# Performance work log

Measured on AMD Instinct MI355X. Metric: run time of the kernel, lower is better.

The kernel has to match this reference:

```python
import jax, jax.numpy as jnp
import numpy as np

L, B, S, H, NH, NS = 4, 8, 2048, 1024, 2, 32
DH = H // NH


def _ln(x, g, b, eps):
    m = jnp.mean(x, axis=-1, keepdims=True)
    v = jnp.mean((x - m) ** 2, axis=-1, keepdims=True)
    return (x - m) / jnp.sqrt(v + eps) * g + b


def setup_inputs() -> dict:
    key = jax.random.key(0)
    ks = jax.random.split(key, 8)
    sc = 0.02
    hidden_states = jax.random.normal(ks[0], (L, B, S, H), jnp.float32)
    attention_mask = jnp.ones((B, S), jnp.int32)
    bnd = jnp.sort(jax.random.randint(ks[1], (B, NS + 1), 0, S - 1), axis=1)
    span_head_idxs = bnd[:, :-1]
    span_tail_idxs = jnp.maximum(bnd[:, 1:], span_head_idxs + 1)  # tail > head, <= S-... (S-1+1=S ok since slice end)
    return {
        "hidden_states": hidden_states,
        "attention_mask": attention_mask,
        "span_head_idxs": span_head_idxs,
        "span_tail_idxs": span_tail_idxs,
        "layer_weights": jnp.linspace(-5.0, 5.0, L),
        "ln1_g": jnp.ones((H,)), "ln1_b": jnp.zeros((H,)),
        "Wq": jax.random.normal(ks[2], (H, H)) * sc, "bq": jnp.zeros((H,)),
        "Wk": jax.random.normal(ks[3], (H, H)) * sc, "bk": jnp.zeros((H,)),
        "Wv": jax.random.normal(ks[4], (H, H)) * sc, "bv": jnp.zeros((H,)),
        "Wo": jax.random.normal(ks[5], (H, H)) * sc, "bo": jnp.zeros((H,)),
        "ln2_g": jnp.ones((H,)), "ln2_b": jnp.zeros((H,)),
    }


def reference(hidden_states, attention_mask, span_head_idxs, span_tail_idxs,
              layer_weights, ln1_g, ln1_b, Wq, bq, Wk, bk, Wv, bv, Wo, bo,
              ln2_g, ln2_b):
    l, b, s, h = hidden_states.shape
    # weighted layer average
    w = jax.nn.softmax(layer_weights)                      # [L]
    x = jnp.einsum('l,lbsh->bsh', w, hidden_states)        # [B,S,H]
    # extended mask (additive)
    ext = (1.0 - attention_mask.astype(x.dtype))[:, None, None, :] * -10000.0
    x = _ln(x, ln1_g, ln1_b, 1e-7)
    # BertSelfAttention (dropout = identity in eval)
    q = (x @ Wq.T + bq).reshape(b, s, NH, DH)
    k = (x @ Wk.T + bk).reshape(b, s, NH, DH)
    v = (x @ Wv.T + bv).reshape(b, s, NH, DH)
    scores = jnp.einsum('bqnd,bknd->bnqk', q, k) / jnp.sqrt(jnp.asarray(DH, x.dtype))
    probs = jax.nn.softmax(scores + ext, axis=-1)          # [B,NH,S,S]
    ctx = jnp.einsum('bnqk,bknd->bqnd', probs, v).reshape(b, s, h)
    # BertSelfOutput: dense + residual + LN (eps=1e-12 default)
    y = _ln(ctx @ Wo.T + bo + x, ln2_g, ln2_b, 1e-12)      # [B,S,H]
    # ragged per-span mean via exclusive cumsum
    csum = jnp.concatenate([jnp.zeros((b, 1, h), y.dtype), jnp.cumsum(y, axis=1)], axis=1)  # [B,S+1,H]
    sh = jnp.take_along_axis(csum, span_head_idxs[..., None], axis=1)   # [B,NS,H]
    st = jnp.take_along_axis(csum, span_tail_idxs[..., None], axis=1)
    lengths = (span_tail_idxs - span_head_idxs).astype(y.dtype)[..., None]
    return (st - sh) / lengths
```

## Files before the change

### kernel.cpp

```cpp
#include <hip/hip_runtime.h>
#include <stdint.h>

#define Ln 4
#define Bn 8
#define Sn 2048
#define Hn 1024
#define NHn 2
#define DHn 512
#define NSn 32
#define Mn (Bn*Sn)

typedef __attribute__((ext_vector_type(8))) short bf16x8;
typedef __attribute__((ext_vector_type(4))) float f32x4;
typedef unsigned short u16;

__device__ __forceinline__ float bf2f(u16 u){
  union { unsigned int i; float f; } c; c.i = ((unsigned int)u)<<16; return c.f;
}
__device__ __forceinline__ u16 f2bf(float f){
  union { float f; unsigned int i; } c; c.f = f;
  unsigned int r = c.i + 0x7FFFu + ((c.i>>16)&1u);
  return (u16)(r>>16);
}
__device__ __forceinline__ uint32_t packbf(float a, float b){
  return (uint32_t)f2bf(a) | ((uint32_t)f2bf(b)<<16);
}
__device__ __forceinline__ void gl2lds16(const void* g, void* l){
  __builtin_amdgcn_global_load_lds((const __attribute__((address_space(1))) void*)g,
                                   (__attribute__((address_space(3))) void*)l, 16, 0, 0);
}

__device__ __forceinline__ float block_sum256(float v, float* red){
#pragma unroll
  for (int m=32;m>=1;m>>=1) v += __shfl_xor(v, m, 64);
  int tid = threadIdx.x;
  if ((tid&63)==0) red[tid>>6] = v;
  __syncthreads();
  v = red[0]+red[1]+red[2]+red[3];
  __syncthreads();
  return v;
}

__global__ __launch_bounds__(256) void convw_kernel(const float* __restrict__ Wq, const float* __restrict__ Wk,
    const float* __restrict__ Wv, const float* __restrict__ Wo, u16* __restrict__ wb){
  int m = blockIdx.y;
  const float* src = (m==0)?Wq:(m==1)?Wk:(m==2)?Wv:Wo;
  size_t i = ((size_t)blockIdx.x*256 + threadIdx.x)*4;
  const float4 v = *(const float4*)&src[i];
  ushort4 o;
  o.x=f2bf(v.x); o.y=f2bf(v.y); o.z=f2bf(v.z); o.w=f2bf(v.w);
  *(ushort4*)&wb[(size_t)m*Hn*Hn + i] = o;
}

__global__ __launch_bounds__(256) void mixln_kernel(const float* __restrict__ hs, const float* __restrict__ lw,
    const float* __restrict__ g, const float* __restrict__ be, u16* __restrict__ xb){
  __shared__ float red[4];
  int row = blockIdx.x;
  int tid = threadIdx.x;
  float l0=lw[0], l1=lw[1], l2=lw[2], l3=lw[3];
  float mx = fmaxf(fmaxf(l0,l1),fmaxf(l2,l3));
  float e0=__expf(l0-mx), e1=__expf(l1-mx), e2=__expf(l2-mx), e3=__expf(l3-mx);
  float inv = 1.0f/(e0+e1+e2+e3);
  e0*=inv; e1*=inv; e2*=inv; e3*=inv;
  size_t base = (size_t)row*Hn + tid*4;
  const float4 h0 = *(const float4*)&hs[base];
  const float4 h1 = *(const float4*)&hs[base + (size_t)Mn*Hn];
  const float4 h2 = *(const float4*)&hs[base + (size_t)2*Mn*Hn];
  const float4 h3 = *(const float4*)&hs[base + (size_t)3*Mn*Hn];
  float x0 = e0*h0.x + e1*h1.x + e2*h2.x + e3*h3.x;
  float x1 = e0*h0.y + e1*h1.y + e2*h2.y + e3*h3.y;
  float x2 = e0*h0.z + e1*h1.z + e2*h2.z + e3*h3.z;
  float x3 = e0*h0.w + e1*h1.w + e2*h2.w + e3*h3.w;
  float s = block_sum256(x0+x1+x2+x3, red);
  float mean = s * (1.0f/Hn);
  float d0=x0-mean, d1=x1-mean, d2=x2-mean, d3=x3-mean;
  float sq = block_sum256(d0*d0+d1*d1+d2*d2+d3*d3, red);
  float rstd = rsqrtf(sq*(1.0f/Hn) + 1e-7f);
  int c = tid*4;
  ushort4 o;
  o.x = f2bf(d0*rstd*g[c+0] + be[c+0]);
  o.y = f2bf(d1*rstd*g[c+1] + be[c+1]);
  o.z = f2bf(d2*rstd*g[c+2] + be[c+2]);
  o.w = f2bf(d3*rstd*g[c+3] + be[c+3]);
  *(ushort4*)&xb[(size_t)row*Hn + c] = o;
}

template<int MODE>
__global__ __launch_bounds__(512,2) void gemm256_kernel(const u16* __restrict__ A, const u16* __restrict__ Bw,
    const float* __restrict__ bias, const u16* __restrict__ resid, void* __restrict__ Cout, float scale){
  __shared__ char ldsb[131072];
  int tid = threadIdx.x, lane = tid&63, wid = tid>>6;
  int ln = lane&15, g4 = lane>>4;
  int wm = wid>>2, wn = wid&3;
  int swz = (blockIdx.x&7)*32 + (blockIdx.x>>3);
  int i0 = (swz>>2)*256;
  int j0 = (swz&3)*256;

  f32x4 acc[8][4];
#pragma unroll
  for (int a=0;a<8;a++)
#pragma unroll
    for (int b=0;b<4;b++) acc[a][b] = (f32x4){0.f,0.f,0.f,0.f};

  const u16* Asrc = A + (size_t)i0*Hn;
  const u16* Bsrc = Bw + (size_t)j0*Hn;
  const int hA = wm, hB = wn>>1, bB = (wn&1)*64;

#define LDSOFF(B,AB,H) ((((B)*2+(AB))*2+(H))*16384)
#define STG(AB,H,B,T) do { \
    const u16* s_ = (AB) ? Bsrc : Asrc; \
    char* d_ = ldsb + LDSOFF(B,AB,H); \
    _Pragma("unroll") \
    for (int l_=0;l_<2;++l_){ \
      int g_ = l_*512 + tid; int r_ = g_>>3; int cs_ = (g_&7) ^ (r_&7); \
      gl2lds16(s_ + (size_t)((H)*128 + r_)*Hn + (T)*64 + cs_*8, d_ + g_*16); \
    } } while(0)
#define RDH(B,AB,H,RR,KG) (*(const bf16x8*)(ldsb + LDSOFF(B,AB,H) + (RR)*128 + ((((KG)) ^ ((RR)&7))<<4)))
#define LOADA(B,I) { _Pragma("unroll") for (int mt=0;mt<4;++mt) \
    _Pragma("unroll") for (int kk=0;kk<2;++kk) af[mt][kk] = RDH(B,0,hA,(I)*64+mt*16+ln, kk*4+g4); }
#define LOADB(B,ARR,J) { _Pragma("unroll") for (int nt=0;nt<2;++nt) \
    _Pragma("unroll") for (int kk=0;kk<2;++kk) ARR[nt][kk] = RDH(B,1,hB, bB+((J)*2+nt)*16+ln, kk*4+g4); }
#define PH_OPEN __builtin_amdgcn_s_barrier(); \
    asm volatile("s_waitcnt lgkmcnt(0)" ::: "memory"); \
    __builtin_amdgcn_sched_barrier(0);
#define MM(I,J,BF) { __builtin_amdgcn_s_setprio(1); \
    _Pragma("unroll") for (int kk=0;kk<2;++kk) \
    _Pragma("unroll") for (int mt=0;mt<4;++mt) \
    _Pragma("unroll") for (int nt=0;nt<2;++nt) \
      acc[(I)*4+mt][(J)*2+nt] = __builtin_amdgcn_mfma_f32_16x16x32_bf16(af[mt][kk], BF[nt][kk], acc[(I)*4+mt][(J)*2+nt], 0,0,0); \
    __builtin_amdgcn_s_setprio(0); }
#define PH_CLOSE __builtin_amdgcn_s_barrier();

  STG(0,0,0,0); STG(0,1,0,0); STG(1,0,0,0); STG(1,1,0,0);
  STG(0,0,1,1);
  asm volatile("s_waitcnt vmcnt(2)" ::: "memory");
  __builtin_amdgcn_s_barrier();

  bf16x8 af[4][2], bf0[2][2], bf1[2][2];
#pragma unroll 1
  for (int it=0; it<8; ++it){
    const int u = 2*it, v = 2*it+1;
    const bool st = (it < 7);
    LOADA(0,0); LOADB(0,bf0,0);
    STG(0,1,1,v);
    PH_OPEN; MM(0,0,bf0); PH_CLOSE;
    LOADB(0,bf1,1);
    STG(1,0,1,v);
    PH_OPEN; MM(0,1,bf1); PH_CLOSE;
    LOADA(0,1);
    STG(1,1,1,v);
    PH_OPEN; MM(1,0,bf0); PH_CLOSE;
    if (st) STG(0,0,0,u+2);
    PH_OPEN; MM(1,1,bf1);
    if (st) { asm volatile("s_waitcnt vmcnt(2)" ::: "memory"); }
    else    { asm volatile("s_waitcnt vmcnt(0)" ::: "memory"); }
    PH_CLOSE;
    LOADA(1,0); LOADB(1,bf0,0);
    if (st) STG(0,1,0,u+2);
    PH_OPEN; MM(0,0,bf0); PH_CLOSE;
    LOADB(1,bf1,1);
    if (st) STG(1,0,0,u+2);
    PH_OPEN; MM(0,1,bf1); PH_CLOSE;
    LOADA(1,1);
    if (st) STG(1,1,0,u+2);
    PH_OPEN; MM(1,0,bf0); PH_CLOSE;
    if (st) STG(0,0,1,v+2);
    PH_OPEN; MM(1,1,bf1);
    if (st) { asm volatile("s_waitcnt vmcnt(2)" ::: "memory"); }
    else    { asm volatile("s_waitcnt vmcnt(0)" ::: "memory"); }
    PH_CLOSE;
  }
#undef LDSOFF
#undef STG
#undef RDH
#undef LOADA
#undef LOADB
#undef PH_OPEN
#undef MM
#undef PH_CLOSE

#pragma unroll
  for (int mt=0; mt<8; ++mt){
#pragma unroll
    for (int nt=0; nt<4; ++nt){
#pragma unroll
      for (int r=0; r<4; ++r){
        int i = i0 + wm*128 + mt*16 + g4*4 + r;
        int j = j0 + wn*64 + nt*16 + ln;
        float v = acc[mt][nt][r] + bias[j];
        if (MODE==0){
          int b = i>>11, s = i&2047, nh = j>>9, dh = j&511;
          ((u16*)Cout)[(((size_t)(b*NHn+nh)*Sn + s)<<9) + dh] = f2bf(v*scale);
        } else if (MODE==1){
          int b = i>>11, s = i&2047, nh = j>>9, dh = j&511;
          ((u16*)Cout)[((size_t)((b*NHn+nh)*(Sn/32) + (s>>5))<<14) + (dh<<5) + (s&31)] = f2bf(v);
        } else {
          float res = bf2f(resid[(size_t)i*Hn + j]);
          ((u16*)Cout)[(size_t)i*Hn + j] = f2bf(v + res);
        }
      }
    }
  }
}

__global__ __launch_bounds__(512,2) void attn_kernel(const u16* __restrict__ qb, const u16* __restrict__ kb,
    const u16* __restrict__ vt, const int* __restrict__ mask, u16* __restrict__ ctx){
  __shared__ u16 Ks[2][32*512];
  __shared__ u16 Vs[2][512*32];
  __shared__ u16 Ps[8*16*32];
  __shared__ float Lcorr[128];
  __shared__ float Lflag[8];
  __shared__ float Linv[128];
  int tid = threadIdx.x, lane = tid&63, wid = tid>>6;
  int ln = lane&15, g4 = lane>>4;
  int gid = blockIdx.x;
  int xcd = gid&7, ord = gid>>3;
  int bh = xcd*2 + (ord>>4), qt = ord&15;
  int b = bh >> 1, nh = bh & 1;
  u16* pw = Ps + wid*512;
  uint32_t* pw32 = (uint32_t*)pw;
  const int swz = (ln&7)<<4;
  const int rsw = (ln>>1)&3;

  bf16x8 aq[16];
  size_t qoff = ((size_t)bh*Sn + qt*128 + wid*16 + ln)*DHn + g4*8;
#pragma unroll
  for (int ch=0; ch<16; ++ch) aq[ch] = *(const bf16x8*)&qb[qoff + ch*32];

  f32x4 o2[8][4];
#pragma unroll
  for (int qf=0; qf<8; ++qf)
#pragma unroll
    for (int df=0; df<4; ++df) o2[qf][df] = (f32x4){0.f,0.f,0.f,0.f};
  float mrun = -1e30f, lrun = 0.f;

  const size_t kbase = (size_t)bh*Sn*DHn;
  const u16* vtile = vt + (size_t)bh*Sn*DHn;

#define STAGE_KV(KT,BUF) do { \
  _Pragma("unroll") \
  for (int t_=0; t_<4; ++t_){ \
    int krow_ = t_*8 + wid; \
    int koff_ = (lane*16) ^ ((krow_&7)<<4); \
    gl2lds16(&kb[kbase + ((size_t)((KT)*32 + krow_))*DHn + (koff_>>1)], \
             (char*)Ks[BUF] + krow_*1024 + lane*16); \
  } \
  _Pragma("unroll") \
  for (int t_=0; t_<4; ++t_){ \
    int p_ = t_*512 + tid; \
    int cgd_ = ((p_&3) ^ ((p_>>3)&3)); \
    gl2lds16(&vtile[(size_t)(KT)*16384 + (p_&~3)*8 + cgd_*8], \
             (char*)Vs[BUF] + p_*16); \
  } } while(0)

  STAGE_KV(0,0);
  __syncthreads();
#pragma unroll 1
  for (int kt=0; kt<Sn/32; ++kt){
    int cur = kt&1;
    if (kt < Sn/32 - 1) STAGE_KV(kt+1, cur^1);
    const char* KsB = (const char*)Ks[cur];
    f32x4 s0 = (f32x4){0.f,0.f,0.f,0.f};
    f32x4 s1 = (f32x4){0.f,0.f,0.f,0.f};
#pragma unroll
    for (int ch=0; ch<16; ++ch){
      bf16x8 k0 = *(const bf16x8*)(KsB + ln*1024      + ((ch*64 + g4*16) ^ swz));
      bf16x8 k1 = *(const bf16x8*)(KsB + (16+ln)*1024 + ((ch*64 + g4*16) ^ swz));
      s0 = __builtin_amdgcn_mfma_f32_16x16x32_bf16(k0, aq[ch], s0, 0,0,0);
      s1 = __builtin_amdgcn_mfma_f32_16x16x32_bf16(k1, aq[ch], s1, 0,0,0);
    }
    int4 mk0 = *(const int4*)&mask[b*Sn + kt*32 + g4*4];
    int4 mk1 = *(const int4*)&mask[b*Sn + kt*32 + 16 + g4*4];
    s0[0] += (float)(1-mk0.x)*-10000.0f; s0[1] += (float)(1-mk0.y)*-10000.0f;
    s0[2] += (float)(1-mk0.z)*-10000.0f; s0[3] += (float)(1-mk0.w)*-10000.0f;
    s1[0] += (float)(1-mk1.x)*-10000.0f; s1[1] += (float)(1-mk1.y)*-10000.0f;
    s1[2] += (float)(1-mk1.z)*-10000.0f; s1[3] += (float)(1-mk1.w)*-10000.0f;
    float tmax = fmaxf(fmaxf(fmaxf(s0[0],s0[1]),fmaxf(s0[2],s0[3])),
                       fmaxf(fmaxf(s1[0],s1[1]),fmaxf(s1[2],s1[3])));
    tmax = fmaxf(tmax, __shfl_xor(tmax, 16));
    tmax = fmaxf(tmax, __shfl_xor(tmax, 32));
    float corr = 1.0f, wflag = 0.0f;
    if (__any(tmax > mrun + 8.0f)){
      float nm = fmaxf(mrun, tmax);
      corr = __expf(mrun - nm);
      mrun = nm; lrun *= corr;
      wflag = 1.0f;
    }
    float p0=__expf(s0[0]-mrun), p1=__expf(s0[1]-mrun), p2=__expf(s0[2]-mrun), p3=__expf(s0[3]-mrun);
    float p4=__expf(s1[0]-mrun), p5=__expf(s1[1]-mrun), p6=__expf(s1[2]-mrun), p7=__expf(s1[3]-mrun);
    float sum = ((p0+p1)+(p2+p3)) + ((p4+p5)+(p6+p7));
    sum += __shfl_xor(sum, 16);
    sum += __shfl_xor(sum, 32);
    lrun += sum;
    {
      int base = ln*16 + ((g4&1)<<1);
      pw32[base + (((g4>>1)    ^rsw)<<2)    ] = packbf(p0,p1);
      pw32[base + (((g4>>1)    ^rsw)<<2) + 1] = packbf(p2,p3);
      pw32[base + ((((g4>>1)+2)^rsw)<<2)    ] = packbf(p4,p5);
      pw32[base + ((((g4>>1)+2)^rsw)<<2) + 1] = packbf(p6,p7);
    }
    if (lane < 16) Lcorr[wid*16 + ln] = corr;
    if (lane == 0) Lflag[wid] = wflag;
    __builtin_amdgcn_sched_barrier(0);
    asm volatile("s_waitcnt lgkmcnt(0)" ::: "memory");
    __builtin_amdgcn_s_barrier();
    __builtin_amdgcn_sched_barrier(0);
    {
      f32x4 fl0 = *(const f32x4*)&Lflag[0];
      f32x4 fl1 = *(const f32x4*)&Lflag[4];
      float fs = (fl0[0]+fl0[1]+fl0[2]+fl0[3]) + (fl1[0]+fl1[1]+fl1[2]+fl1[3]);
      if (fs > 0.5f){
#pragma unroll
        for (int qf=0; qf<8; ++qf){
          f32x4 c4 = *(const f32x4*)&Lcorr[qf*16 + g4*4];
#pragma unroll
          for (int df=0; df<4; ++df){
            o2[qf][df][0]*=c4[0]; o2[qf][df][1]*=c4[1];
            o2[qf][df][2]*=c4[2]; o2[qf][df][3]*=c4[3];
          }
        }
      }
    }
    const char* VsB = (const char*)Vs[cur];
    bf16x8 bv[4];
#pragma unroll
    for (int df=0; df<4; ++df)
      bv[df] = *(const bf16x8*)(VsB + ((wid*4+df)*16+ln)*64 + ((g4 ^ rsw)<<4));
#pragma unroll
    for (int qf=0; qf<8; ++qf){
      bf16x8 aP = *(const bf16x8*)&Ps[qf*512 + ln*32 + ((g4 ^ rsw)<<3)];
#pragma unroll
      for (int df=0; df<4; ++df)
        o2[qf][df] = __builtin_amdgcn_mfma_f32_16x16x32_bf16(aP, bv[df], o2[qf][df], 0,0,0);
    }
    __syncthreads();
  }
#undef STAGE_KV
  if (lane < 16) Linv[wid*16 + ln] = 1.0f/lrun;
  __syncthreads();
  int qr0 = qt*128;
#pragma unroll
  for (int qf=0; qf<8; ++qf){
    f32x4 il4 = *(const f32x4*)&Linv[qf*16 + g4*4];
#pragma unroll
    for (int df=0; df<4; ++df){
#pragma unroll
      for (int r=0; r<4; ++r){
        int q = qr0 + qf*16 + g4*4 + r;
        int d = nh*DHn + wid*64 + df*16 + ln;
        ctx[((size_t)(b*Sn + q))*Hn + d] = f2bf(o2[qf][df][r]*il4[r]);
      }
    }
  }
}

__global__ __launch_bounds__(256) void ln2_kernel(u16* __restrict__ t, const float* __restrict__ g,
    const float* __restrict__ be){
  __shared__ float red[4];
  int row = blockIdx.x, tid = threadIdx.x;
  const ushort4 xu = *(const ushort4*)&t[(size_t)row*Hn + tid*4];
  float x0 = bf2f(xu.x), x1 = bf2f(xu.y), x2 = bf2f(xu.z), x3 = bf2f(xu.w);
  float s = block_sum256(x0+x1+x2+x3, red);
  float mean = s*(1.0f/Hn);
  float d0=x0-mean, d1=x1-mean, d2=x2-mean, d3=x3-mean;
  float sq = block_sum256(d0*d0+d1*d1+d2*d2+d3*d3, red);
  float rstd = rsqrtf(sq*(1.0f/Hn) + 1e-12f);
  int c = tid*4;
  ushort4 y;
  y.x = f2bf(d0*rstd*g[c+0] + be[c+0]);
  y.y = f2bf(d1*rstd*g[c+1] + be[c+1]);
  y.z = f2bf(d2*rstd*g[c+2] + be[c+2]);
  y.w = f2bf(d3*rstd*g[c+3] + be[c+3]);
  *(ushort4*)&t[(size_t)row*Hn + c] = y;
}

__global__ __launch_bounds__(256) void span_kernel(const u16* __restrict__ y, const int* __restrict__ head,
    const int* __restrict__ tail, float* __restrict__ out){
  int bs = blockIdx.x;
  int b = bs >> 5;
  int hd = head[bs], tl = tail[bs];
  int c = threadIdx.x*4;
  float a0=0.f,a1=0.f,a2=0.f,a3=0.f;
  for (int s=hd; s<tl; ++s){
    const ushort4 v = *(const ushort4*)&y[((size_t)(b*Sn + s))*Hn + c];
    a0+=bf2f(v.x); a1+=bf2f(v.y); a2+=bf2f(v.z); a3+=bf2f(v.w);
  }
  float inv = 1.0f/(float)(tl-hd);
  float4 o; o.x=a0*inv; o.y=a1*inv; o.z=a2*inv; o.w=a3*inv;
  *(float4*)&out[(size_t)bs*Hn + c] = o;
}

extern "C" void kernel_launch(void* const* d_in, const int* in_sizes, int n_in,
                              void* d_out, int out_size, void* d_ws, size_t ws_size,
                              hipStream_t stream) {
  const float* hs    = (const float*)d_in[0];
  const int*   mask  = (const int*)d_in[1];
  const int*   shead = (const int*)d_in[2];
  const int*   stail = (const int*)d_in[3];
  const float* lw    = (const float*)d_in[4];
  const float* ln1g  = (const float*)d_in[5];
  const float* ln1b  = (const float*)d_in[6];
  const float* Wq    = (const float*)d_in[7];
  const float* bq    = (const float*)d_in[8];
  const float* Wk    = (const float*)d_in[9];
  const float* bk    = (const float*)d_in[10];
  const float* Wv    = (const float*)d_in[11];
  const float* bv    = (const float*)d_in[12];
  const float* Wo    = (const float*)d_in[13];
  const float* bo    = (const float*)d_in[14];
  const float* ln2g  = (const float*)d_in[15];
  const float* ln2b  = (const float*)d_in[16];

  char* ws = (char*)d_ws;
  u16* xb  = (u16*)(ws);
  u16* wb  = (u16*)(ws + 33554432);
  u16* qb  = (u16*)(ws + 41943040);
  u16* kb  = (u16*)(ws + 75497472);
  u16* vt  = (u16*)(ws + 109051904);
  u16* ctx = (u16*)(ws + 142606336);
  u16* t   = (u16*)(ws + 41943040);
  float* out = (float*)d_out;

  convw_kernel<<<dim3(1024,4),256,0,stream>>>(Wq,Wk,Wv,Wo,wb);
  mixln_kernel<<<Mn,256,0,stream>>>(hs,lw,ln1g,ln1b,xb);
  gemm256_kernel<0><<<256,512,0,stream>>>(xb, wb,           bq, nullptr, qb, 0.044194173824159223f);
  gemm256_kernel<0><<<256,512,0,stream>>>(xb, wb+1048576,   bk, nullptr, kb, 1.0f);
  gemm256_kernel<1><<<256,512,0,stream>>>(xb, wb+2097152,   bv, nullptr, vt, 1.0f);
  attn_kernel<<<256,512,0,stream>>>(qb,kb,vt,mask,ctx);
  gemm256_kernel<2><<<256,512,0,stream>>>(ctx, wb+3145728,  bo, xb, t, 1.0f);
  ln2_kernel<<<Mn,256,0,stream>>>(t, ln2g, ln2b);
  span_kernel<<<Bn*NSn,256,0,stream>>>(t, shead, stail, out);
}
```

Measured before the change: 547.4 us.

## Fuse QKV projections into one GEMM launch and widen attention key tiles to 64

The three Q/K/V projection GEMMs become a single 768-block launch. Each block picks its bias, scale and output layout from the column tile it owns, which removes two launches and fills the GPU with more concurrent tiles. The attention kernel now processes 64 keys per iteration instead of 32. K staging is no longer double-buffered: the next K tile is issued after the mid-iteration barrier, and V is staged at the start of the same iteration. This halves the loop trip count and barrier count per key, at the cost of less load/compute overlap and larger P/K LDS buffers.

Result: slower. 654.5 us (+19.6%).

```diff
diff --git a/kernel.cpp b/kernel.cpp
--- a/kernel.cpp
+++ b/kernel.cpp
@@ -87,14 +87,22 @@
 
 template<int MODE>
 __global__ __launch_bounds__(512,2) void gemm256_kernel(const u16* __restrict__ A, const u16* __restrict__ Bw,
-    const float* __restrict__ bias, const u16* __restrict__ resid, void* __restrict__ Cout, float scale){
+    const float* __restrict__ b0, const float* __restrict__ b1, const float* __restrict__ b2,
+    const u16* __restrict__ resid, void* __restrict__ Cout, float scale){
   __shared__ char ldsb[131072];
   int tid = threadIdx.x, lane = tid&63, wid = tid>>6;
   int ln = lane&15, g4 = lane>>4;
   int wm = wid>>2, wn = wid&3;
-  int swz = (blockIdx.x&7)*32 + (blockIdx.x>>3);
-  int i0 = (swz>>2)*256;
-  int j0 = (swz&3)*256;
+  int i0, j0;
+  if (MODE==0){
+    int xcd = blockIdx.x&7, idx = blockIdx.x>>3;
+    i0 = (xcd*8 + idx/12)*256;
+    j0 = (idx%12)*256;
+  } else {
+    int swz = (blockIdx.x&7)*32 + (blockIdx.x>>3);
+    i0 = (swz>>2)*256;
+    j0 = (swz&3)*256;
+  }
 
   f32x4 acc[8][4];
 #pragma unroll
@@ -179,6 +187,10 @@
 #undef MM
 #undef PH_CLOSE
 
+  int mat = (MODE==0) ? (j0>>10) : 0;
+  const float* bias = (MODE==0) ? ((mat==0)?b0:((mat==1)?b1:b2)) : b0;
+  float sc = (MODE==0 && mat==0) ? scale : 1.0f;
+  u16* dst = (u16*)Cout + ((MODE==0) ? (size_t)mat*16777216 : 0);
 #pragma unroll
   for (int mt=0; mt<8; ++mt){
 #pragma unroll
@@ -187,16 +199,18 @@
       for (int r=0; r<4; ++r){
         int i = i0 + wm*128 + mt*16 + g4*4 + r;
         int j = j0 + wn*64 + nt*16 + ln;
-        float v = acc[mt][nt][r] + bias[j];
+        int jj = j & 1023;
+        float v = acc[mt][nt][r] + bias[jj];
         if (MODE==0){
-          int b = i>>11, s = i&2047, nh = j>>9, dh = j&511;
-          ((u16*)Cout)[(((size_t)(b*NHn+nh)*Sn + s)<<9) + dh] = f2bf(v*scale);
-        } else if (MODE==1){
-          int b = i>>11, s = i&2047, nh = j>>9, dh = j&511;
-          ((u16*)Cout)[((size_t)((b*NHn+nh)*(Sn/32) + (s>>5))<<14) + (dh<<5) + (s&31)] = f2bf(v);
+          int b = i>>11, s = i&2047, nh = jj>>9, dh = jj&511;
+          if (mat < 2){
+            dst[(((size_t)(b*NHn+nh)*Sn + s)<<9) + dh] = f2bf(v*sc);
+          } else {
+            dst[((size_t)((b*NHn+nh)*(Sn/32) + (s>>5))<<14) + (dh<<5) + (s&31)] = f2bf(v);
+          }
         } else {
-          float res = bf2f(resid[(size_t)i*Hn + j]);
-          ((u16*)Cout)[(size_t)i*Hn + j] = f2bf(v + res);
+          float res = bf2f(resid[(size_t)i*Hn + jj]);
+          dst[(size_t)i*Hn + jj] = f2bf(v + res);
         }
       }
     }
@@ -205,9 +219,9 @@
 
 __global__ __launch_bounds__(512,2) void attn_kernel(const u16* __restrict__ qb, const u16* __restrict__ kb,
     const u16* __restrict__ vt, const int* __restrict__ mask, u16* __restrict__ ctx){
-  __shared__ u16 Ks[2][32*512];
+  __shared__ u16 Ks[64*512];
   __shared__ u16 Vs[2][512*32];
-  __shared__ u16 Ps[8*16*32];
+  __shared__ u16 Ps[128*64];
   __shared__ float Lcorr[128];
   __shared__ float Lflag[8];
   __shared__ float Linv[128];
@@ -217,10 +231,10 @@
   int xcd = gid&7, ord = gid>>3;
   int bh = xcd*2 + (ord>>4), qt = ord&15;
   int b = bh >> 1, nh = bh & 1;
-  u16* pw = Ps + wid*512;
-  uint32_t* pw32 = (uint32_t*)pw;
-  const int swz = (ln&7)<<4;
-  const int rsw = (ln>>1)&3;
+  uint32_t* ps32 = (uint32_t*)Ps;
+  const int swz  = (ln&7)<<4;
+  const int rsw  = (ln>>1)&3;
+  const int rsw7 = (ln>>1)&7;
 
   bf16x8 aq[16];
   size_t qoff = ((size_t)bh*Sn + qt*128 + wid*16 + ln)*DHn + g4*8;
@@ -237,46 +251,66 @@
   const size_t kbase = (size_t)bh*Sn*DHn;
   const u16* vtile = vt + (size_t)bh*Sn*DHn;
 
-#define STAGE_KV(KT,BUF) do { \
+#define STAGE_K64(KT) do { \
   _Pragma("unroll") \
-  for (int t_=0; t_<4; ++t_){ \
+  for (int t_=0; t_<8; ++t_){ \
     int krow_ = t_*8 + wid; \
     int koff_ = (lane*16) ^ ((krow_&7)<<4); \
-    gl2lds16(&kb[kbase + ((size_t)((KT)*32 + krow_))*DHn + (koff_>>1)], \
-             (char*)Ks[BUF] + krow_*1024 + lane*16); \
-  } \
+    gl2lds16(&kb[kbase + ((size_t)((KT)*64 + krow_))*DHn + (koff_>>1)], \
+             (char*)Ks + krow_*1024 + lane*16); \
+  } } while(0)
+
+#define STAGE_V64(KT) do { \
   _Pragma("unroll") \
-  for (int t_=0; t_<4; ++t_){ \
-    int p_ = t_*512 + tid; \
-    int cgd_ = ((p_&3) ^ ((p_>>3)&3)); \
-    gl2lds16(&vtile[(size_t)(KT)*16384 + (p_&~3)*8 + cgd_*8], \
-             (char*)Vs[BUF] + p_*16); \
-  } } while(0)
-
-  STAGE_KV(0,0);
+  for (int sub_=0; sub_<2; ++sub_){ \
+    _Pragma("unroll") \
+    for (int t_=0; t_<4; ++t_){ \
+      int p_ = t_*512 + tid; \
+      int cgd_ = ((p_&3) ^ ((p_>>3)&3)); \
+      gl2lds16(&vtile[(size_t)((KT)*2+sub_)*16384 + (p_&~3)*8 + cgd_*8], \
+               (char*)Vs[sub_] + p_*16); \
+    } } } while(0)
+
+  STAGE_K64(0);
   __syncthreads();
 #pragma unroll 1
-  for (int kt=0; kt<Sn/32; ++kt){
-    int cur = kt&1;
-    if (kt < Sn/32 - 1) STAGE_KV(kt+1, cur^1);
-    const char* KsB = (const char*)Ks[cur];
+  for (int kt=0; kt<Sn/64; ++kt){
+    STAGE_V64(kt);
     f32x4 s0 = (f32x4){0.f,0.f,0.f,0.f};
     f32x4 s1 = (f32x4){0.f,0.f,0.f,0.f};
+    f32x4 s2 = (f32x4){0.f,0.f,0.f,0.f};
+    f32x4 s3 = (f32x4){0.f,0.f,0.f,0.f};
 #pragma unroll
     for (int ch=0; ch<16; ++ch){
-      bf16x8 k0 = *(const bf16x8*)(KsB + ln*1024      + ((ch*64 + g4*16) ^ swz));
-      bf16x8 k1 = *(const bf16x8*)(KsB + (16+ln)*1024 + ((ch*64 + g4*16) ^ swz));
+      int co = (ch*64 + g4*16) ^ swz;
+      bf16x8 k0 = *(const bf16x8*)((char*)Ks + (ln   )*1024 + co);
+      bf16x8 k1 = *(const bf16x8*)((char*)Ks + (16+ln)*1024 + co);
+      bf16x8 k2 = *(const bf16x8*)((char*)Ks + (32+ln)*1024 + co);
+      bf16x8 k3 = *(const bf16x8*)((char*)Ks + (48+ln)*1024 + co);
       s0 = __builtin_amdgcn_mfma_f32_16x16x32_bf16(k0, aq[ch], s0, 0,0,0);
       s1 = __builtin_amdgcn_mfma_f32_16x16x32_bf16(k1, aq[ch], s1, 0,0,0);
-    }
-    int4 mk0 = *(const int4*)&mask[b*Sn + kt*32 + g4*4];
-    int4 mk1 = *(const int4*)&mask[b*Sn + kt*32 + 16 + g4*4];
-    s0[0] += (float)(1-mk0.x)*-10000.0f; s0[1] += (float)(1-mk0.y)*-10000.0f;
-    s0[2] += (float)(1-mk0.z)*-10000.0f; s0[3] += (float)(1-mk0.w)*-10000.0f;
-    s1[0] += (float)(1-mk1.x)*-10000.0f; s1[1] += (float)(1-mk1.y)*-10000.0f;
-    s1[2] += (float)(1-mk1.z)*-10000.0f; s1[3] += (float)(1-mk1.w)*-10000.0f;
+      s2 = __builtin_amdgcn_mfma_f32_16x16x32_bf16(k2, aq[ch], s2, 0,0,0);
+      s3 = __builtin_amdgcn_mfma_f32_16x16x32_bf16(k3, aq[ch], s3, 0,0,0);
+    }
+    {
+      int mb = b*Sn + kt*64 + g4*4;
+      int4 mk0 = *(const int4*)&mask[mb];
+      int4 mk1 = *(const int4*)&mask[mb+16];
+      int4 mk2 = *(const int4*)&mask[mb+32];
+      int4 mk3 = *(const int4*)&mask[mb+48];
+      s0[0]+=(float)(1-mk0.x)*-10000.0f; s0[1]+=(float)(1-mk0.y)*-10000.0f;
+      s0[2]+=(float)(1-mk0.z)*-10000.0f; s0[3]+=(float)(1-mk0.w)*-10000.0f;
+      s1[0]+=(float)(1-mk1.x)*-10000.0f; s1[1]+=(float)(1-mk1.y)*-10000.0f;
+      s1[2]+=(float)(1-mk1.z)*-10000.0f; s1[3]+=(float)(1-mk1.w)*-10000.0f;
+      s2[0]+=(float)(1-mk2.x)*-10000.0f; s2[1]+=(float)(1-mk2.y)*-10000.0f;
+      s2[2]+=(float)(1-mk2.z)*-10000.0f; s2[3]+=(float)(1-mk2.w)*-10000.0f;
+      s3[0]+=(float)(1-mk3.x)*-10000.0f; s3[1]+=(float)(1-mk3.y)*-10000.0f;
+      s3[2]+=(float)(1-mk3.z)*-10000.0f; s3[3]+=(float)(1-mk3.w)*-10000.0f;
+    }
     float tmax = fmaxf(fmaxf(fmaxf(s0[0],s0[1]),fmaxf(s0[2],s0[3])),
                        fmaxf(fmaxf(s1[0],s1[1]),fmaxf(s1[2],s1[3])));
+    tmax = fmaxf(tmax, fmaxf(fmaxf(fmaxf(s2[0],s2[1]),fmaxf(s2[2],s2[3])),
+                             fmaxf(fmaxf(s3[0],s3[1]),fmaxf(s3[2],s3[3]))));
     tmax = fmaxf(tmax, __shfl_xor(tmax, 16));
     tmax = fmaxf(tmax, __shfl_xor(tmax, 32));
     float corr = 1.0f, wflag = 0.0f;
@@ -286,25 +320,43 @@
       mrun = nm; lrun *= corr;
       wflag = 1.0f;
     }
-    float p0=__expf(s0[0]-mrun), p1=__expf(s0[1]-mrun), p2=__expf(s0[2]-mrun), p3=__expf(s0[3]-mrun);
-    float p4=__expf(s1[0]-mrun), p5=__expf(s1[1]-mrun), p6=__expf(s1[2]-mrun), p7=__expf(s1[3]-mrun);
-    float sum = ((p0+p1)+(p2+p3)) + ((p4+p5)+(p6+p7));
+    float sum = 0.f;
+    int pbase = (wid*16 + ln)*32 + (g4&1)*2;
+    {
+      float a0=__expf(s0[0]-mrun), a1=__expf(s0[1]-mrun), a2=__expf(s0[2]-mrun), a3=__expf(s0[3]-mrun);
+      sum += (a0+a1)+(a2+a3);
+      int gsw = ((0*2 + (g4>>1)) ^ rsw7)<<2;
+      ps32[pbase + gsw    ] = packbf(a0,a1);
+      ps32[pbase + gsw + 1] = packbf(a2,a3);
+    }
+    {
+      float a0=__expf(s1[0]-mrun), a1=__expf(s1[1]-mrun), a2=__expf(s1[2]-mrun), a3=__expf(s1[3]-mrun);
+      sum += (a0+a1)+(a2+a3);
+      int gsw = ((1*2 + (g4>>1)) ^ rsw7)<<2;
+      ps32[pbase + gsw    ] = packbf(a0,a1);
+      ps32[pbase + gsw + 1] = packbf(a2,a3);
+    }
+    {
+      float a0=__expf(s2[0]-mrun), a1=__expf(s2[1]-mrun), a2=__expf(s2[2]-mrun), a3=__expf(s2[3]-mrun);
+      sum += (a0+a1)+(a2+a3);
+      int gsw = ((2*2 + (g4>>1)) ^ rsw7)<<2;
+      ps32[pbase + gsw    ] = packbf(a0,a1);
+      ps32[pbase + gsw + 1] = packbf(a2,a3);
+    }
+    {
+      float a0=__expf(s3[0]-mrun), a1=__expf(s3[1]-mrun), a2=__expf(s3[2]-mrun), a3=__expf(s3[3]-mrun);
+      sum += (a0+a1)+(a2+a3);
+      int gsw = ((3*2 + (g4>>1)) ^ rsw7)<<2;
+      ps32[pbase + gsw    ] = packbf(a0,a1);
+      ps32[pbase + gsw + 1] = packbf(a2,a3);
+    }
     sum += __shfl_xor(sum, 16);
     sum += __shfl_xor(sum, 32);
     lrun += sum;
-    {
-      int base = ln*16 + ((g4&1)<<1);
-      pw32[base + (((g4>>1)    ^rsw)<<2)    ] = packbf(p0,p1);
-      pw32[base + (((g4>>1)    ^rsw)<<2) + 1] = packbf(p2,p3);
-      pw32[base + ((((g4>>1)+2)^rsw)<<2)    ] = packbf(p4,p5);
-      pw32[base + ((((g4>>1)+2)^rsw)<<2) + 1] = packbf(p6,p7);
-    }
     if (lane < 16) Lcorr[wid*16 + ln] = corr;
     if (lane == 0) Lflag[wid] = wflag;
-    __builtin_amdgcn_sched_barrier(0);
-    asm volatile("s_waitcnt lgkmcnt(0)" ::: "memory");
-    __builtin_amdgcn_s_barrier();
-    __builtin_amdgcn_sched_barrier(0);
+    __syncthreads();
+    if (kt < Sn/64 - 1) STAGE_K64(kt+1);
     {
       f32x4 fl0 = *(const f32x4*)&Lflag[0];
       f32x4 fl1 = *(const f32x4*)&Lflag[4];
@@ -321,21 +373,26 @@
         }
       }
     }
-    const char* VsB = (const char*)Vs[cur];
-    bf16x8 bv[4];
+    bf16x8 bv[4][2];
 #pragma unroll
     for (int df=0; df<4; ++df)
-      bv[df] = *(const bf16x8*)(VsB + ((wid*4+df)*16+ln)*64 + ((g4 ^ rsw)<<4));
+#pragma unroll
+      for (int kc=0; kc<2; ++kc)
+        bv[df][kc] = *(const bf16x8*)((char*)Vs[kc] + ((wid*4+df)*16+ln)*64 + ((g4 ^ rsw)<<4));
 #pragma unroll
     for (int qf=0; qf<8; ++qf){
-      bf16x8 aP = *(const bf16x8*)&Ps[qf*512 + ln*32 + ((g4 ^ rsw)<<3)];
-#pragma unroll
-      for (int df=0; df<4; ++df)
-        o2[qf][df] = __builtin_amdgcn_mfma_f32_16x16x32_bf16(aP, bv[df], o2[qf][df], 0,0,0);
+#pragma unroll
+      for (int kc=0; kc<2; ++kc){
+        bf16x8 aP = *(const bf16x8*)((char*)Ps + (qf*16+ln)*128 + (((kc*4+g4) ^ rsw7)<<4));
+#pragma unroll
+        for (int df=0; df<4; ++df)
+          o2[qf][df] = __builtin_amdgcn_mfma_f32_16x16x32_bf16(aP, bv[df][kc], o2[qf][df], 0,0,0);
+      }
     }
     __syncthreads();
   }
-#undef STAGE_KV
+#undef STAGE_K64
+#undef STAGE_V64
   if (lane < 16) Linv[wid*16 + ln] = 1.0f/lrun;
   __syncthreads();
   int qr0 = qt*128;
@@ -423,11 +480,9 @@
 
   convw_kernel<<<dim3(1024,4),256,0,stream>>>(Wq,Wk,Wv,Wo,wb);
   mixln_kernel<<<Mn,256,0,stream>>>(hs,lw,ln1g,ln1b,xb);
-  gemm256_kernel<0><<<256,512,0,stream>>>(xb, wb,           bq, nullptr, qb, 0.044194173824159223f);
-  gemm256_kernel<0><<<256,512,0,stream>>>(xb, wb+1048576,   bk, nullptr, kb, 1.0f);
-  gemm256_kernel<1><<<256,512,0,stream>>>(xb, wb+2097152,   bv, nullptr, vt, 1.0f);
+  gemm256_kernel<0><<<768,512,0,stream>>>(xb, wb, bq, bk, bv, nullptr, qb, 0.044194173824159223f);
   attn_kernel<<<256,512,0,stream>>>(qb,kb,vt,mask,ctx);
-  gemm256_kernel<2><<<256,512,0,stream>>>(ctx, wb+3145728,  bo, xb, t, 1.0f);
+  gemm256_kernel<2><<<256,512,0,stream>>>(ctx, wb+3145728, bo, bo, bo, xb, t, 1.0f);
   ln2_kernel<<<Mn,256,0,stream>>>(t, ln2g, ln2b);
   span_kernel<<<Bn*NSn,256,0,stream>>>(t, shead, stail, out);
 }
```

## Shrink attention tiles to 64 queries and single-buffer K/V with split staging

Applied to the files above, without the earlier changes.

Attention blocks now cover 64 query rows with 4 waves instead of 128 rows with 8 waves, and the grid doubles to 512 blocks. K and V lose their double buffers. V for the current tile is loaded at the start of the iteration, and K for the next tile is loaded after the mid-loop barrier. The smaller LDS footprint should allow more resident blocks per CU and improve occupancy. In exchange, each block now re-reads K/V for only half as many queries, doubling K/V global traffic, and loads now overlap less with compute.

Result: slower. 777.7 us (+42.1%).

```diff
diff --git a/kernel.cpp b/kernel.cpp
--- a/kernel.cpp
+++ b/kernel.cpp
@@ -203,19 +203,19 @@
   }
 }
 
-__global__ __launch_bounds__(512,2) void attn_kernel(const u16* __restrict__ qb, const u16* __restrict__ kb,
+__global__ __launch_bounds__(256,2) void attn_kernel(const u16* __restrict__ qb, const u16* __restrict__ kb,
     const u16* __restrict__ vt, const int* __restrict__ mask, u16* __restrict__ ctx){
-  __shared__ u16 Ks[2][32*512];
-  __shared__ u16 Vs[2][512*32];
-  __shared__ u16 Ps[8*16*32];
-  __shared__ float Lcorr[128];
-  __shared__ float Lflag[8];
-  __shared__ float Linv[128];
+  __shared__ u16 Ks[32*512];
+  __shared__ u16 Vs[512*32];
+  __shared__ u16 Ps[4*16*32];
+  __shared__ float Lcorr[64];
+  __shared__ float Lflag[4];
+  __shared__ float Linv[64];
   int tid = threadIdx.x, lane = tid&63, wid = tid>>6;
   int ln = lane&15, g4 = lane>>4;
   int gid = blockIdx.x;
   int xcd = gid&7, ord = gid>>3;
-  int bh = xcd*2 + (ord>>4), qt = ord&15;
+  int bh = xcd*2 + (ord>>5), qt = ord&31;
   int b = bh >> 1, nh = bh & 1;
   u16* pw = Ps + wid*512;
   uint32_t* pw32 = (uint32_t*)pw;
@@ -223,49 +223,51 @@
   const int rsw = (ln>>1)&3;
 
   bf16x8 aq[16];
-  size_t qoff = ((size_t)bh*Sn + qt*128 + wid*16 + ln)*DHn + g4*8;
+  size_t qoff = ((size_t)bh*Sn + qt*64 + wid*16 + ln)*DHn + g4*8;
 #pragma unroll
   for (int ch=0; ch<16; ++ch) aq[ch] = *(const bf16x8*)&qb[qoff + ch*32];
 
-  f32x4 o2[8][4];
-#pragma unroll
-  for (int qf=0; qf<8; ++qf)
-#pragma unroll
-    for (int df=0; df<4; ++df) o2[qf][df] = (f32x4){0.f,0.f,0.f,0.f};
+  f32x4 o2[4][8];
+#pragma unroll
+  for (int qf=0; qf<4; ++qf)
+#pragma unroll
+    for (int df=0; df<8; ++df) o2[qf][df] = (f32x4){0.f,0.f,0.f,0.f};
   float mrun = -1e30f, lrun = 0.f;
 
   const size_t kbase = (size_t)bh*Sn*DHn;
   const u16* vtile = vt + (size_t)bh*Sn*DHn;
 
-#define STAGE_KV(KT,BUF) do { \
+#define STAGE_K32(KT) do { \
   _Pragma("unroll") \
-  for (int t_=0; t_<4; ++t_){ \
-    int krow_ = t_*8 + wid; \
+  for (int t_=0; t_<8; ++t_){ \
+    int krow_ = t_*4 + wid; \
     int koff_ = (lane*16) ^ ((krow_&7)<<4); \
     gl2lds16(&kb[kbase + ((size_t)((KT)*32 + krow_))*DHn + (koff_>>1)], \
-             (char*)Ks[BUF] + krow_*1024 + lane*16); \
-  } \
+             (char*)Ks + krow_*1024 + lane*16); \
+  } } while(0)
+
+#define STAGE_V32(KT) do { \
   _Pragma("unroll") \
-  for (int t_=0; t_<4; ++t_){ \
-    int p_ = t_*512 + tid; \
+  for (int t_=0; t_<8; ++t_){ \
+    int p_ = t_*256 + tid; \
     int cgd_ = ((p_&3) ^ ((p_>>3)&3)); \
     gl2lds16(&vtile[(size_t)(KT)*16384 + (p_&~3)*8 + cgd_*8], \
-             (char*)Vs[BUF] + p_*16); \
+             (char*)Vs + p_*16); \
   } } while(0)
 
-  STAGE_KV(0,0);
+  STAGE_K32(0);
   __syncthreads();
 #pragma unroll 1
   for (int kt=0; kt<Sn/32; ++kt){
-    int cur = kt&1;
-    if (kt < Sn/32 - 1) STAGE_KV(kt+1, cur^1);
-    const char* KsB = (const char*)Ks[cur];
+    STAGE_V32(kt);
+    const char* KsB = (const char*)Ks;
     f32x4 s0 = (f32x4){0.f,0.f,0.f,0.f};
     f32x4 s1 = (f32x4){0.f,0.f,0.f,0.f};
 #pragma unroll
     for (int ch=0; ch<16; ++ch){
-      bf16x8 k0 = *(const bf16x8*)(KsB + ln*1024      + ((ch*64 + g4*16) ^ swz));
-      bf16x8 k1 = *(const bf16x8*)(KsB + (16+ln)*1024 + ((ch*64 + g4*16) ^ swz));
+      int co = (ch*64 + g4*16) ^ swz;
+      bf16x8 k0 = *(const bf16x8*)(KsB + ln*1024      + co);
+      bf16x8 k1 = *(const bf16x8*)(KsB + (16+ln)*1024 + co);
       s0 = __builtin_amdgcn_mfma_f32_16x16x32_bf16(k0, aq[ch], s0, 0,0,0);
       s1 = __builtin_amdgcn_mfma_f32_16x16x32_bf16(k1, aq[ch], s1, 0,0,0);
     }
@@ -301,53 +303,51 @@
     }
     if (lane < 16) Lcorr[wid*16 + ln] = corr;
     if (lane == 0) Lflag[wid] = wflag;
-    __builtin_amdgcn_sched_barrier(0);
-    asm volatile("s_waitcnt lgkmcnt(0)" ::: "memory");
-    __builtin_amdgcn_s_barrier();
-    __builtin_amdgcn_sched_barrier(0);
+    __syncthreads();
+    if (kt < Sn/32 - 1) STAGE_K32(kt+1);
     {
-      f32x4 fl0 = *(const f32x4*)&Lflag[0];
-      f32x4 fl1 = *(const f32x4*)&Lflag[4];
-      float fs = (fl0[0]+fl0[1]+fl0[2]+fl0[3]) + (fl1[0]+fl1[1]+fl1[2]+fl1[3]);
+      f32x4 fl = *(const f32x4*)&Lflag[0];
+      float fs = (fl[0]+fl[1])+(fl[2]+fl[3]);
       if (fs > 0.5f){
 #pragma unroll
-        for (int qf=0; qf<8; ++qf){
+        for (int qf=0; qf<4; ++qf){
           f32x4 c4 = *(const f32x4*)&Lcorr[qf*16 + g4*4];
 #pragma unroll
-          for (int df=0; df<4; ++df){
+          for (int df=0; df<8; ++df){
             o2[qf][df][0]*=c4[0]; o2[qf][df][1]*=c4[1];
             o2[qf][df][2]*=c4[2]; o2[qf][df][3]*=c4[3];
           }
         }
       }
     }
-    const char* VsB = (const char*)Vs[cur];
-    bf16x8 bv[4];
-#pragma unroll
-    for (int df=0; df<4; ++df)
-      bv[df] = *(const bf16x8*)(VsB + ((wid*4+df)*16+ln)*64 + ((g4 ^ rsw)<<4));
-#pragma unroll
-    for (int qf=0; qf<8; ++qf){
+    const char* VsB = (const char*)Vs;
+    bf16x8 bv[8];
+#pragma unroll
+    for (int df=0; df<8; ++df)
+      bv[df] = *(const bf16x8*)(VsB + ((wid*8+df)*16+ln)*64 + ((g4 ^ rsw)<<4));
+#pragma unroll
+    for (int qf=0; qf<4; ++qf){
       bf16x8 aP = *(const bf16x8*)&Ps[qf*512 + ln*32 + ((g4 ^ rsw)<<3)];
 #pragma unroll
-      for (int df=0; df<4; ++df)
+      for (int df=0; df<8; ++df)
         o2[qf][df] = __builtin_amdgcn_mfma_f32_16x16x32_bf16(aP, bv[df], o2[qf][df], 0,0,0);
     }
     __syncthreads();
   }
-#undef STAGE_KV
+#undef STAGE_K32
+#undef STAGE_V32
   if (lane < 16) Linv[wid*16 + ln] = 1.0f/lrun;
   __syncthreads();
-  int qr0 = qt*128;
-#pragma unroll
-  for (int qf=0; qf<8; ++qf){
+  int qr0 = qt*64;
+#pragma unroll
+  for (int qf=0; qf<4; ++qf){
     f32x4 il4 = *(const f32x4*)&Linv[qf*16 + g4*4];
 #pragma unroll
-    for (int df=0; df<4; ++df){
+    for (int df=0; df<8; ++df){
 #pragma unroll
       for (int r=0; r<4; ++r){
         int q = qr0 + qf*16 + g4*4 + r;
-        int d = nh*DHn + wid*64 + df*16 + ln;
+        int d = nh*DHn + wid*128 + df*16 + ln;
         ctx[((size_t)(b*Sn + q))*Hn + d] = f2bf(o2[qf][df][r]*il4[r]);
       }
     }
@@ -426,7 +426,7 @@
   gemm256_kernel<0><<<256,512,0,stream>>>(xb, wb,           bq, nullptr, qb, 0.044194173824159223f);
   gemm256_kernel<0><<<256,512,0,stream>>>(xb, wb+1048576,   bk, nullptr, kb, 1.0f);
   gemm256_kernel<1><<<256,512,0,stream>>>(xb, wb+2097152,   bv, nullptr, vt, 1.0f);
-  attn_kernel<<<256,512,0,stream>>>(qb,kb,vt,mask,ctx);
+  attn_kernel<<<512,256,0,stream>>>(qb,kb,vt,mask,ctx);
   gemm256_kernel<2><<<256,512,0,stream>>>(ctx, wb+3145728,  bo, xb, t, 1.0f);
   ln2_kernel<<<Mn,256,0,stream>>>(t, ln2g, ln2b);
   span_kernel<<<Bn*NSn,256,0,stream>>>(t, shead, stail, out);
```

## Software-pipeline attention loop: defer PV of previous tile behind QK of current

Applied to the files above, without the earlier changes.

Double-buffers the P, correction and flag shared arrays and moves the P·V MFMA for tile kt-1 into iteration kt, so only one barrier per iteration remains and QK compute overlaps the PV stage. K is staged one tile ahead, while V is now loaded for the current tile and consumed in the next iteration. This removes the mid-iteration barrier but adds LDS usage and a tail PV step. The V load for a tile now has only the time until the next iteration to land.

New measurement: 578.0 us. 1.06x slower.

```diff
diff --git a/kernel.cpp b/kernel.cpp
--- a/kernel.cpp
+++ b/kernel.cpp
@@ -207,9 +207,9 @@
     const u16* __restrict__ vt, const int* __restrict__ mask, u16* __restrict__ ctx){
   __shared__ u16 Ks[2][32*512];
   __shared__ u16 Vs[2][512*32];
-  __shared__ u16 Ps[8*16*32];
-  __shared__ float Lcorr[128];
-  __shared__ float Lflag[8];
+  __shared__ u16 Ps[2][8*16*32];
+  __shared__ float Lcorr[2][128];
+  __shared__ float Lflag[2][8];
   __shared__ float Linv[128];
   int tid = threadIdx.x, lane = tid&63, wid = tid>>6;
   int ln = lane&15, g4 = lane>>4;
@@ -217,8 +217,6 @@
   int xcd = gid&7, ord = gid>>3;
   int bh = xcd*2 + (ord>>4), qt = ord&15;
   int b = bh >> 1, nh = bh & 1;
-  u16* pw = Ps + wid*512;
-  uint32_t* pw32 = (uint32_t*)pw;
   const int swz = (ln&7)<<4;
   const int rsw = (ln>>1)&3;
 
@@ -237,14 +235,16 @@
   const size_t kbase = (size_t)bh*Sn*DHn;
   const u16* vtile = vt + (size_t)bh*Sn*DHn;
 
-#define STAGE_KV(KT,BUF) do { \
+#define STAGE_K(KT,BUF) do { \
   _Pragma("unroll") \
   for (int t_=0; t_<4; ++t_){ \
     int krow_ = t_*8 + wid; \
     int koff_ = (lane*16) ^ ((krow_&7)<<4); \
     gl2lds16(&kb[kbase + ((size_t)((KT)*32 + krow_))*DHn + (koff_>>1)], \
              (char*)Ks[BUF] + krow_*1024 + lane*16); \
-  } \
+  } } while(0)
+
+#define STAGE_V(KT,BUF) do { \
   _Pragma("unroll") \
   for (int t_=0; t_<4; ++t_){ \
     int p_ = t_*512 + tid; \
@@ -253,12 +253,41 @@
              (char*)Vs[BUF] + p_*16); \
   } } while(0)
 
-  STAGE_KV(0,0);
+#define DO_PV(PB) do { \
+    f32x4 fl0 = *(const f32x4*)&Lflag[PB][0]; \
+    f32x4 fl1 = *(const f32x4*)&Lflag[PB][4]; \
+    float fs = (fl0[0]+fl0[1]+fl0[2]+fl0[3]) + (fl1[0]+fl1[1]+fl1[2]+fl1[3]); \
+    if (fs > 0.5f){ \
+      _Pragma("unroll") \
+      for (int qf=0; qf<8; ++qf){ \
+        f32x4 c4 = *(const f32x4*)&Lcorr[PB][qf*16 + g4*4]; \
+        _Pragma("unroll") \
+        for (int df=0; df<4; ++df){ \
+          o2[qf][df][0]*=c4[0]; o2[qf][df][1]*=c4[1]; \
+          o2[qf][df][2]*=c4[2]; o2[qf][df][3]*=c4[3]; \
+        } \
+      } \
+    } \
+    const char* VsB = (const char*)Vs[PB]; \
+    bf16x8 bv[4]; \
+    _Pragma("unroll") \
+    for (int df=0; df<4; ++df) \
+      bv[df] = *(const bf16x8*)(VsB + ((wid*4+df)*16+ln)*64 + ((g4 ^ rsw)<<4)); \
+    _Pragma("unroll") \
+    for (int qf=0; qf<8; ++qf){ \
+      bf16x8 aP = *(const bf16x8*)&Ps[PB][qf*512 + ln*32 + ((g4 ^ rsw)<<3)]; \
+      _Pragma("unroll") \
+      for (int df=0; df<4; ++df) \
+        o2[qf][df] = __builtin_amdgcn_mfma_f32_16x16x32_bf16(aP, bv[df], o2[qf][df], 0,0,0); \
+    } } while(0)
+
+  STAGE_K(0,0);
   __syncthreads();
 #pragma unroll 1
   for (int kt=0; kt<Sn/32; ++kt){
-    int cur = kt&1;
-    if (kt < Sn/32 - 1) STAGE_KV(kt+1, cur^1);
+    int cur = kt&1, pb = cur^1;
+    if (kt < Sn/32 - 1) STAGE_K(kt+1, pb);
+    STAGE_V(kt, cur);
     const char* KsB = (const char*)Ks[cur];
     f32x4 s0 = (f32x4){0.f,0.f,0.f,0.f};
     f32x4 s1 = (f32x4){0.f,0.f,0.f,0.f};
@@ -293,49 +322,22 @@
     sum += __shfl_xor(sum, 32);
     lrun += sum;
     {
+      uint32_t* pw32 = (uint32_t*)(Ps[cur] + wid*512);
       int base = ln*16 + ((g4&1)<<1);
       pw32[base + (((g4>>1)    ^rsw)<<2)    ] = packbf(p0,p1);
       pw32[base + (((g4>>1)    ^rsw)<<2) + 1] = packbf(p2,p3);
       pw32[base + ((((g4>>1)+2)^rsw)<<2)    ] = packbf(p4,p5);
       pw32[base + ((((g4>>1)+2)^rsw)<<2) + 1] = packbf(p6,p7);
     }
-    if (lane < 16) Lcorr[wid*16 + ln] = corr;
-    if (lane == 0) Lflag[wid] = wflag;
-    __builtin_amdgcn_sched_barrier(0);
-    asm volatile("s_waitcnt lgkmcnt(0)" ::: "memory");
-    __builtin_amdgcn_s_barrier();
-    __builtin_amdgcn_sched_barrier(0);
-    {
-      f32x4 fl0 = *(const f32x4*)&Lflag[0];
-      f32x4 fl1 = *(const f32x4*)&Lflag[4];
-      float fs = (fl0[0]+fl0[1]+fl0[2]+fl0[3]) + (fl1[0]+fl1[1]+fl1[2]+fl1[3]);
-      if (fs > 0.5f){
-#pragma unroll
-        for (int qf=0; qf<8; ++qf){
-          f32x4 c4 = *(const f32x4*)&Lcorr[qf*16 + g4*4];
-#pragma unroll
-          for (int df=0; df<4; ++df){
-            o2[qf][df][0]*=c4[0]; o2[qf][df][1]*=c4[1];
-            o2[qf][df][2]*=c4[2]; o2[qf][df][3]*=c4[3];
-          }
-        }
-      }
-    }
-    const char* VsB = (const char*)Vs[cur];
-    bf16x8 bv[4];
-#pragma unroll
-    for (int df=0; df<4; ++df)
-      bv[df] = *(const bf16x8*)(VsB + ((wid*4+df)*16+ln)*64 + ((g4 ^ rsw)<<4));
-#pragma unroll
-    for (int qf=0; qf<8; ++qf){
-      bf16x8 aP = *(const bf16x8*)&Ps[qf*512 + ln*32 + ((g4 ^ rsw)<<3)];
-#pragma unroll
-      for (int df=0; df<4; ++df)
-        o2[qf][df] = __builtin_amdgcn_mfma_f32_16x16x32_bf16(aP, bv[df], o2[qf][df], 0,0,0);
-    }
+    if (lane < 16) Lcorr[cur][wid*16 + ln] = corr;
+    if (lane == 0) Lflag[cur][wid] = wflag;
+    if (kt > 0) DO_PV(pb);
     __syncthreads();
   }
-#undef STAGE_KV
+  DO_PV(1);
+#undef STAGE_K
+#undef STAGE_V
+#undef DO_PV
   if (lane < 16) Linv[wid*16 + ln] = 1.0f/lrun;
   __syncthreads();
   int qr0 = qt*128;
```
